# Kernel tuning notes

Hardware: AMD Instinct MI355X
Metric: run time of the kernel (lower is better)

Reference implementation:

```python
import jax, jax.numpy as jnp
import numpy as np

D_MODEL = 1024
D_STATE = 256

def setup_inputs() -> dict:
    key = jax.random.key(0)
    k1, k2, k3, k4 = jax.random.split(key, 4)
    x = jax.random.normal(k1, (8, 4096, D_MODEL), dtype=jnp.float32)
    A = jax.random.normal(k2, (D_STATE,), dtype=jnp.float32)
    B = jax.random.normal(k3, (D_STATE, D_MODEL), dtype=jnp.float32) * 0.01
    C = jax.random.normal(k4, (D_MODEL, D_STATE), dtype=jnp.float32) * 0.01
    D = jnp.ones((D_MODEL,), dtype=jnp.float32)
    return {"x": x, "A": A, "B": B, "C": C, "D": D}

def reference(x, A, B, C, D):
    # x: (b, s, d_model)
    a_bar = jnp.exp(-jnp.exp(A))                     # (n,)
    Bx = jnp.einsum('bsd,nd->bsn', x, B)             # (b, s, n) precomputed input drive

    def step(h, bx_t):
        h = a_bar * h + bx_t                          # (b, n)
        return h, h

    h0 = jnp.zeros((x.shape[0], A.shape[0]), dtype=x.dtype)
    # scan over time axis: move seq to leading axis
    _, hs = jax.lax.scan(step, h0, jnp.swapaxes(Bx, 0, 1))  # hs: (s, b, n)
    hs = jnp.swapaxes(hs, 0, 1)                      # (b, s, n)
    y = jnp.einsum('bsn,dn->bsd', hs, C) + D * x     # (b, s, d_model)
    return y
```

## Files before the change

### kernel.cpp

```cpp
#include <hip/hip_runtime.h>
#include <cstdint>
#include <cstddef>


typedef __attribute__((ext_vector_type(8))) _Float16 half8;
typedef __attribute__((ext_vector_type(4))) float f32x4;

__device__ inline half8 cvt8(float4 a, float4 b) {
  half8 h;
  h[0] = (_Float16)a.x; h[1] = (_Float16)a.y;
  h[2] = (_Float16)a.z; h[3] = (_Float16)a.w;
  h[4] = (_Float16)b.x; h[5] = (_Float16)b.y;
  h[6] = (_Float16)b.z; h[7] = (_Float16)b.w;
  return h;
}

__global__ __launch_bounds__(256) void cvt_bc(
    const float* __restrict__ Bp, const float* __restrict__ Cp,
    _Float16* __restrict__ Bh, _Float16* __restrict__ Ch)
{
  const int g = blockIdx.x * 256 + threadIdx.x;
  const size_t off = (size_t)(g & 32767) * 8;
  const float* src = (g < 32768) ? (Bp + off) : (Cp + off);
  _Float16*    dst = (g < 32768) ? (Bh + off) : (Ch + off);
  float4 a = *(const float4*)src;
  float4 b = *(const float4*)(src + 4);
  *(half8*)dst = cvt8(a, b);
}

__global__ __launch_bounds__(256) void gemm_bx(
    const float* __restrict__ x, const _Float16* __restrict__ Bh,
    const float* __restrict__ Ap,
    _Float16* __restrict__ Bxh, float* __restrict__ E)
{
  __shared__ _Float16 lb[256 * 128];

  const int tid  = threadIdx.x;
  const int lane = tid & 63;
  const int wave = tid >> 6;
  const int quad = lane >> 4;
  const int l16  = lane & 15;
  const long blockM = (long)blockIdx.x * 64;
  const long arow = blockM + wave * 16 + l16;

  f32x4 acc[16];
  #pragma unroll
  for (int i = 0; i < 16; i++) acc[i] = (f32x4){0.f, 0.f, 0.f, 0.f};

  for (int kc = 0; kc < 8; kc++) {
    __syncthreads();
    {
      const int n = tid;
      const _Float16* src = Bh + (size_t)n * 1024 + kc * 128;
      #pragma unroll
      for (int j = 0; j < 16; j++) {
        half8 v = *(const half8*)(src + j * 8);
        const int k8p = j ^ (n & 7);
        *(half8*)&lb[n * 128 + k8p * 8] = v;
      }
    }
    half8 af[4];
    #pragma unroll
    for (int ks = 0; ks < 4; ks++) {
      const float* ga = x + arow * 1024 + kc * 128 + ks * 32 + quad * 8;
      float4 a0 = *(const float4*)ga;
      float4 a1 = *(const float4*)(ga + 4);
      af[ks] = cvt8(a0, a1);
    }
    __syncthreads();
    #pragma unroll
    for (int ks = 0; ks < 4; ks++) {
      #pragma unroll
      for (int nt = 0; nt < 16; nt++) {
        const int n   = nt * 16 + l16;
        const int k8p = (ks * 4 + quad) ^ (n & 7);
        half8 bf = *(const half8*)&lb[n * 128 + k8p * 8];
        acc[nt] = __builtin_amdgcn_mfma_f32_16x16x32_f16(af[ks], bf, acc[nt], 0, 0, 0);
      }
    }
  }

  __syncthreads();
  #pragma unroll
  for (int nt = 0; nt < 16; nt++)
    #pragma unroll
    for (int r = 0; r < 4; r++)
      lb[(wave * 16 + quad * 4 + r) * 256 + nt * 16 + l16] = (_Float16)acc[nt][r];
  __syncthreads();
  {
    const int row = tid >> 2, seg = tid & 3;
    _Float16* dst = Bxh + (blockM + row) * 256 + seg * 64;
    const _Float16* srcl = &lb[row * 256 + seg * 64];
    #pragma unroll
    for (int j = 0; j < 8; j++)
      *(half8*)(dst + j * 8) = *(const half8*)(srcl + j * 8);
  }
  {
    const float al = expf(-expf(Ap[tid]));
    float h = 0.f;
    #pragma unroll 8
    for (int t = 0; t < 64; t++)
      h = fmaf(al, h, (float)lb[t * 256 + tid]);
    E[(size_t)blockIdx.x * 256 + tid] = h;
  }
}

__global__ __launch_bounds__(256) void scan_prefix(
    const float* __restrict__ E, const float* __restrict__ Ap,
    float* __restrict__ carry)
{
  __shared__ float4 se4[4096];
  const int n = threadIdx.x;
  const int b = blockIdx.x;

  const float4* src4 = (const float4*)(E + (size_t)b * 64 * 256);
  #pragma unroll
  for (int j = 0; j < 16; j++)
    se4[j * 256 + n] = src4[j * 256 + n];

  const float al = expf(-expf(Ap[n]));
  float aL = al;
  #pragma unroll
  for (int i = 0; i < 6; i++) aL *= aL;

  __syncthreads();
  const float* se = (const float*)se4;
  float run = 0.f;
  for (int c = 0; c < 64; c++) {
    carry[((size_t)b * 64 + c) * 256 + n] = run;
    run = fmaf(aL, run, se[c * 256 + n]);
  }
}

__global__ __launch_bounds__(256) void scan_apply(
    _Float16* __restrict__ Bxh, const float* __restrict__ Ap,
    const float* __restrict__ carry)
{
  const int n  = threadIdx.x;
  const int bc = blockIdx.x;
  const float al = expf(-expf(Ap[n]));
  float h = carry[(size_t)bc * 256 + n];
  const size_t base = (size_t)bc * 64 * 256 + n;
  #pragma unroll 16
  for (int t = 0; t < 64; t++) {
    const size_t i = base + (size_t)t * 256;
    h = fmaf(al, h, (float)Bxh[i]);
    Bxh[i] = (_Float16)h;
  }
}

__global__ __launch_bounds__(256, 3) void gemm_y(
    const _Float16* __restrict__ hs, const _Float16* __restrict__ Ch,
    const float* __restrict__ x, const float* __restrict__ Dp,
    float* __restrict__ y)
{
  __shared__ _Float16 lc[64 * 256];

  const int tid  = threadIdx.x;
  const int lane = tid & 63;
  const int wave = tid >> 6;
  const int quad = lane >> 4;
  const int l16  = lane & 15;
  const int slab = blockIdx.x & 15;
  const int mg   = blockIdx.x >> 4;
  const int n0   = slab * 64;

  {
    const int n = tid >> 2, q = tid & 3;
    const _Float16* src = Ch + (size_t)(n0 + n) * 256 + q * 64;
    #pragma unroll
    for (int j = 0; j < 8; j++) {
      half8 v = *(const half8*)(src + j * 8);
      const int k8p = (q * 8 + j) ^ (n & 7);
      *(half8*)&lc[n * 256 + k8p * 8] = v;
    }
  }
  __syncthreads();

  auto load_chunk = [&](int i, half8* af, float4* xv) {
    const long row = ((long)mg * 4 + i) * 64 + wave * 16 + l16;
    const _Float16* ph = hs + row * 256;
    #pragma unroll
    for (int ks = 0; ks < 8; ks++)
      af[ks] = *(const half8*)(ph + ks * 32 + quad * 8);
    const float* px = x + row * 1024 + n0 + quad * 4;
    #pragma unroll
    for (int nt = 0; nt < 4; nt++)
      xv[nt] = *(const float4*)(px + nt * 16);
  };

  auto compute_chunk = [&](int i, const half8* af, const float4* xv) {
    const long row = ((long)mg * 4 + i) * 64 + wave * 16 + l16;
    f32x4 acc[4];
    #pragma unroll
    for (int nt = 0; nt < 4; nt++) acc[nt] = (f32x4){0.f, 0.f, 0.f, 0.f};

    #pragma unroll
    for (int ks = 0; ks < 8; ks++) {
      #pragma unroll
      for (int nt = 0; nt < 4; nt++) {
        const int n   = nt * 16 + l16;
        const int k8p = (ks * 4 + quad) ^ (n & 7);
        half8 cf = *(const half8*)&lc[n * 256 + k8p * 8];
        acc[nt] = __builtin_amdgcn_mfma_f32_16x16x32_f16(cf, af[ks], acc[nt], 0, 0, 0);
      }
    }

    float* py = y + row * 1024 + n0 + quad * 4;
    const float* pD = Dp + n0 + quad * 4;
    #pragma unroll
    for (int nt = 0; nt < 4; nt++) {
      float4 dv = *(const float4*)(pD + nt * 16);
      float4 o;
      o.x = acc[nt][0] + dv.x * xv[nt].x;
      o.y = acc[nt][1] + dv.y * xv[nt].y;
      o.z = acc[nt][2] + dv.z * xv[nt].z;
      o.w = acc[nt][3] + dv.w * xv[nt].w;
      *(float4*)(py + nt * 16) = o;
    }
  };

  half8 afA[8], afB[8];
  float4 xvA[4], xvB[4];
  load_chunk(0, afA, xvA);
  load_chunk(1, afB, xvB);
  compute_chunk(0, afA, xvA);
  load_chunk(2, afA, xvA);
  compute_chunk(1, afB, xvB);
  load_chunk(3, afB, xvB);
  compute_chunk(2, afA, xvA);
  compute_chunk(3, afB, xvB);
}

extern "C" void kernel_launch(void* const* d_in, const int* in_sizes, int n_in,
                              void* d_out, int out_size, void* d_ws, size_t ws_size,
                              hipStream_t stream) {
  const float* x  = (const float*)d_in[0];
  const float* Ap = (const float*)d_in[1];
  const float* Bp = (const float*)d_in[2];
  const float* Cp = (const float*)d_in[3];
  const float* Dp = (const float*)d_in[4];
  float* y = (float*)d_out;

  _Float16* Bxh = (_Float16*)d_ws;
  _Float16* Bh  = Bxh + (size_t)32768 * 256;
  _Float16* Ch  = Bh + (size_t)256 * 1024;
  float* E      = (float*)(Ch + (size_t)1024 * 256);
  float* carry  = E + (size_t)512 * 256;

  cvt_bc     <<<256,  256, 0, stream>>>(Bp, Cp, Bh, Ch);
  gemm_bx    <<<512,  256, 0, stream>>>(x, Bh, Ap, Bxh, E);
  scan_prefix<<<8,    256, 0, stream>>>(E, Ap, carry);
  scan_apply <<<512,  256, 0, stream>>>(Bxh, Ap, carry);
  gemm_y     <<<2048, 256, 0, stream>>>(Bxh, Ch, x, Dp, y);
}
```

Before: 328.6 us.

## Restructure gemm_y to keep hs rows in registers and loop over C slabs

gemm_y now assigns each block 64 rows and half of the output columns. The block loads its hs fragments once into registers, then iterates over 8 column slabs of C, refilling shared memory for each slab. Before, each block held one C slab and walked 4 row chunks with software pipelining. The aim is to cut redundant hs reads: each hs row was read 16 times and is now read twice. In exchange, C slab reloads go into LDS every iteration with extra barriers, the x loads are no longer double-buffered, and launch bounds rise to 4 blocks per SM.

```diff
diff --git a/kernel.cpp b/kernel.cpp
--- a/kernel.cpp
+++ b/kernel.cpp
@@ -149,7 +149,7 @@
   }
 }
 
-__global__ __launch_bounds__(256, 3) void gemm_y(
+__global__ __launch_bounds__(256, 4) void gemm_y(
     const _Float16* __restrict__ hs, const _Float16* __restrict__ Ch,
     const float* __restrict__ x, const float* __restrict__ Dp,
     float* __restrict__ y)
@@ -161,36 +161,45 @@
   const int wave = tid >> 6;
   const int quad = lane >> 4;
   const int l16  = lane & 15;
-  const int slab = blockIdx.x & 15;
-  const int mg   = blockIdx.x >> 4;
-  const int n0   = slab * 64;
-
+  const int cg   = blockIdx.x & 1;
+  const long mg  = blockIdx.x >> 1;
+  const long row = mg * 64 + wave * 16 + l16;
+
+  half8 af[8];
   {
-    const int n = tid >> 2, q = tid & 3;
-    const _Float16* src = Ch + (size_t)(n0 + n) * 256 + q * 64;
-    #pragma unroll
-    for (int j = 0; j < 8; j++) {
-      half8 v = *(const half8*)(src + j * 8);
-      const int k8p = (q * 8 + j) ^ (n & 7);
-      *(half8*)&lc[n * 256 + k8p * 8] = v;
-    }
-  }
-  __syncthreads();
-
-  auto load_chunk = [&](int i, half8* af, float4* xv) {
-    const long row = ((long)mg * 4 + i) * 64 + wave * 16 + l16;
     const _Float16* ph = hs + row * 256;
     #pragma unroll
     for (int ks = 0; ks < 8; ks++)
       af[ks] = *(const half8*)(ph + ks * 32 + quad * 8);
+  }
+
+  const int nfill = tid >> 2, qfill = tid & 3;
+
+  for (int it = 0; it < 8; it++) {
+    const int n0 = cg * 512 + it * 64;
+
+    if (it) __syncthreads();
+    {
+      const _Float16* src = Ch + (size_t)(n0 + nfill) * 256 + qfill * 64;
+      #pragma unroll
+      for (int j = 0; j < 8; j++) {
+        half8 v = *(const half8*)(src + j * 8);
+        const int k8p = (qfill * 8 + j) ^ (nfill & 7);
+        *(half8*)&lc[nfill * 256 + k8p * 8] = v;
+      }
+    }
+
     const float* px = x + row * 1024 + n0 + quad * 4;
-    #pragma unroll
-    for (int nt = 0; nt < 4; nt++)
+    const float* pD = Dp + n0 + quad * 4;
+    float4 xv[4], dv[4];
+    #pragma unroll
+    for (int nt = 0; nt < 4; nt++) {
       xv[nt] = *(const float4*)(px + nt * 16);
-  };
-
-  auto compute_chunk = [&](int i, const half8* af, const float4* xv) {
-    const long row = ((long)mg * 4 + i) * 64 + wave * 16 + l16;
+      dv[nt] = *(const float4*)(pD + nt * 16);
+    }
+
+    __syncthreads();
+
     f32x4 acc[4];
     #pragma unroll
     for (int nt = 0; nt < 4; nt++) acc[nt] = (f32x4){0.f, 0.f, 0.f, 0.f};
@@ -199,37 +208,24 @@
     for (int ks = 0; ks < 8; ks++) {
       #pragma unroll
       for (int nt = 0; nt < 4; nt++) {
-        const int n   = nt * 16 + l16;
-        const int k8p = (ks * 4 + quad) ^ (n & 7);
-        half8 cf = *(const half8*)&lc[n * 256 + k8p * 8];
+        const int nl  = nt * 16 + l16;
+        const int k8p = (ks * 4 + quad) ^ (nl & 7);
+        half8 cf = *(const half8*)&lc[nl * 256 + k8p * 8];
         acc[nt] = __builtin_amdgcn_mfma_f32_16x16x32_f16(cf, af[ks], acc[nt], 0, 0, 0);
       }
     }
 
     float* py = y + row * 1024 + n0 + quad * 4;
-    const float* pD = Dp + n0 + quad * 4;
     #pragma unroll
     for (int nt = 0; nt < 4; nt++) {
-      float4 dv = *(const float4*)(pD + nt * 16);
       float4 o;
-      o.x = acc[nt][0] + dv.x * xv[nt].x;
-      o.y = acc[nt][1] + dv.y * xv[nt].y;
-      o.z = acc[nt][2] + dv.z * xv[nt].z;
-      o.w = acc[nt][3] + dv.w * xv[nt].w;
+      o.x = acc[nt][0] + dv[nt].x * xv[nt].x;
+      o.y = acc[nt][1] + dv[nt].y * xv[nt].y;
+      o.z = acc[nt][2] + dv[nt].z * xv[nt].z;
+      o.w = acc[nt][3] + dv[nt].w * xv[nt].w;
       *(float4*)(py + nt * 16) = o;
     }
-  };
-
-  half8 afA[8], afB[8];
-  float4 xvA[4], xvB[4];
-  load_chunk(0, afA, xvA);
-  load_chunk(1, afB, xvB);
-  compute_chunk(0, afA, xvA);
-  load_chunk(2, afA, xvA);
-  compute_chunk(1, afB, xvB);
-  load_chunk(3, afB, xvB);
-  compute_chunk(2, afA, xvA);
-  compute_chunk(3, afB, xvB);
+  }
 }
 
 extern "C" void kernel_launch(void* const* d_in, const int* in_sizes, int n_in,
@@ -252,5 +248,5 @@
   gemm_bx    <<<512,  256, 0, stream>>>(x, Bh, Ap, Bxh, E);
   scan_prefix<<<8,    256, 0, stream>>>(E, Ap, carry);
   scan_apply <<<512,  256, 0, stream>>>(Bxh, Ap, carry);
-  gemm_y     <<<2048, 256, 0, stream>>>(Bxh, Ch, x, Dp, y);
-}
+  gemm_y     <<<1024, 256, 0, stream>>>(Bxh, Ch, x, Dp, y);
+}
```

New measurement: 323.1 us. Within noise of the previous version (-1.7%).
